# Kernel tuning notes

Hardware: AMD Instinct MI355X
Metric: run time of the kernel (lower is better)

Reference implementation:

```python
import jax, jax.numpy as jnp
import numpy as np

# Dims
B_, L_, IN_ = 16, 8192, 57
DM, DS, HD, EXP, NL, OUT = 64, 32, 32, 2, 2, 6
DI = EXP * DM            # 128 inner dim
NH = DI // HD            # 4 heads
DPROJ = 2 * DI + 2 * DS + NH  # z, x, B, C, dt


def setup_inputs() -> dict:
    key = jax.random.key(0)
    ks = jax.random.split(key, 8)
    def rn(k, shape, scale=0.02):
        return jax.random.normal(k, shape, dtype=jnp.float32) * scale
    return {
        "x": jax.random.normal(ks[0], (B_, L_, IN_), dtype=jnp.float32),
        "W_in": rn(ks[1], (IN_, DM)),
        "b_in": jnp.zeros((DM,), jnp.float32),
        "in_proj_W": rn(ks[2], (NL, DM, DPROJ)),
        "in_proj_b": jnp.zeros((NL, DPROJ), jnp.float32),
        "A_log": jnp.log(jnp.broadcast_to(jnp.arange(1, NH + 1, dtype=jnp.float32), (NL, NH))),
        "D": jnp.ones((NL, NH), jnp.float32),
        "dt_bias": rn(ks[3], (NL, NH), 0.1),
        "out_proj_W": rn(ks[4], (NL, DI, DM)),
        "out_proj_b": jnp.zeros((NL, DM), jnp.float32),
        "cls_W": rn(ks[5], (DM, OUT)),
        "cls_b": jnp.zeros((OUT,), jnp.float32),
    }


def _mamba_layer(x, W, b, A_log, D, dt_bias, Wo, bo):
    """SISO Mamba3-style selective scan block. x: [B, L, DM]."""
    Bsz, L, _ = x.shape
    zxbcdt = x @ W + b                               # [B, L, DPROJ]
    z, xin, Bm, Cm, dt = jnp.split(
        zxbcdt, [DI, 2 * DI, 2 * DI + DS, 2 * DI + 2 * DS], axis=-1)
    dt = jax.nn.softplus(dt + dt_bias)               # [B, L, NH]
    A = -jnp.exp(A_log)                              # [NH], per-head scalar (SISO)
    xin = jax.nn.silu(xin).reshape(Bsz, L, NH, HD)   # [B, L, NH, HD]
    Bm = jax.nn.silu(Bm)                             # [B, L, DS]
    Cm = jax.nn.silu(Cm)                             # [B, L, DS]
    decay = jnp.exp(dt * A)                          # [B, L, NH]

    def step(h, inp):
        # h: [B, NH, HD, DS]
        xt, bt, ct, dtt, dect = inp
        h = dect[:, :, None, None] * h + (dtt[:, :, None] * xt)[..., None] * bt[:, None, None, :]
        yt = jnp.einsum('bhpn,bn->bhp', h, ct)       # [B, NH, HD]
        return h, yt

    h0 = jnp.zeros((Bsz, NH, HD, DS), x.dtype)
    xs = (jnp.moveaxis(xin, 1, 0), jnp.moveaxis(Bm, 1, 0), jnp.moveaxis(Cm, 1, 0),
          jnp.moveaxis(dt, 1, 0), jnp.moveaxis(decay, 1, 0))
    _, ys = jax.lax.scan(step, h0, xs)               # [L, B, NH, HD]
    y = jnp.moveaxis(ys, 0, 1) + D[None, None, :, None] * xin
    y = y.reshape(Bsz, L, DI) * jax.nn.silu(z)       # gated output
    return y @ Wo + bo                               # [B, L, DM]


def reference(x, W_in, b_in, in_proj_W, in_proj_b, A_log, D, dt_bias,
              out_proj_W, out_proj_b, cls_W, cls_b):
    h = x @ W_in + b_in                              # linear_in
    for l in range(NL):                              # residual Mamba stack
        h = h + _mamba_layer(h, in_proj_W[l], in_proj_b[l], A_log[l], D[l],
                             dt_bias[l], out_proj_W[l], out_proj_b[l])
    pooled = h.mean(axis=1)                          # AdaptiveAvgPool1d(1)
    return pooled @ cls_W + cls_b                    # classifier [B, OUT]
```

## Files before the change

kernel.cpp:

```cpp
#include <hip/hip_runtime.h>

#define BSZ   16
#define LSEQ  8192
#define DMDL  64
#define DSD   32
#define HDD   32
#define NHD   4
#define DIN   128
#define NLAY  2
#define NOUTC 6
#define DPRJ  324
#define QC    64
#define NCH   128
#define NT21  21

typedef __attribute__((ext_vector_type(8))) short bf16x8;
typedef __attribute__((ext_vector_type(4))) float f32x4;

__device__ float          g_h0[BSZ*LSEQ*DMDL];
__device__ unsigned short g_xy[BSZ*LSEQ*DIN];
__device__ unsigned short g_Ca[BSZ*LSEQ*DSD];
__device__ float          g_pc[BSZ*LSEQ*NHD];
__device__ unsigned short g_cS[BSZ*NCH*NHD*HDD*DSD];
__device__ unsigned short g_Hb[BSZ*NCH*NHD*HDD*DSD];
__device__ float          g_cL[BSZ*NCH*NHD];
__device__ float          g_ppc[BSZ*NCH*DMDL];
__device__ unsigned short g_wf[NLAY*NT21*2*64*8];
__device__ unsigned short g_wo[NLAY*4*4*64*8];

__device__ __forceinline__ float silu_f(float v){ return v / (1.0f + __expf(-v)); }
__device__ __forceinline__ float softplus_f(float v){ return (v > 15.0f) ? v : __logf(1.0f + __expf(v)); }
__device__ __forceinline__ unsigned short f2bf(float f){
  union { float f; unsigned u; } v; v.f = f;
  unsigned r = v.u + 0x7FFFu + ((v.u >> 16) & 1u);
  return (unsigned short)(r >> 16);
}
__device__ __forceinline__ float bf2f(unsigned short h){
  union { unsigned u; float f; } v; v.u = ((unsigned)h) << 16;
  return v.f;
}
__device__ __forceinline__ unsigned cvtpk(float lo, float hi){
  unsigned r;
  asm("v_cvt_pk_bf16_f32 %0, %1, %2" : "=v"(r) : "v"(lo), "v"(hi));
  return r;
}

#define LSTR 132
__global__ __launch_bounds__(256) void k_linin(
    const float* __restrict__ x, const float* __restrict__ W,
    const float* __restrict__ bias)
{
  __shared__ float xt[57*LSTR];
  __shared__ float wl[57*64];
  const int tid = threadIdx.x;
  const long tb = (long)blockIdx.x * 128;
  for (int i = tid; i < 912; i += 256)
    *(float4*)&wl[i*4] = *(const float4*)&W[i*4];
  for (int i = tid; i < 1824; i += 256){
    float4 v = *(const float4*)&x[tb*57 + (long)i*4];
    const int e = i*4;
    int t0 = e / 57;
    int k0 = e - t0*57;
    float vv[4] = {v.x, v.y, v.z, v.w};
    #pragma unroll
    for (int j = 0; j < 4; ++j){
      int t = t0, k = k0 + j;
      if (k >= 57){ t += 1; k -= 57; }
      xt[k*LSTR + t] = vv[j];
    }
  }
  __syncthreads();
  const int d0 = (tid & 7) * 8;
  const int t0 = (tid >> 3) * 4;
  float acc[4][8];
  #pragma unroll
  for (int i = 0; i < 4; ++i)
    #pragma unroll
    for (int j = 0; j < 8; ++j) acc[i][j] = 0.f;
  #pragma unroll 4
  for (int k = 0; k < 57; ++k){
    float4 xv4 = *(const float4*)&xt[k*LSTR + t0];
    float4 w0  = *(const float4*)&wl[k*64 + d0];
    float4 w1  = *(const float4*)&wl[k*64 + d0 + 4];
    float xv[4] = {xv4.x, xv4.y, xv4.z, xv4.w};
    float wv[8] = {w0.x, w0.y, w0.z, w0.w, w1.x, w1.y, w1.z, w1.w};
    #pragma unroll
    for (int i = 0; i < 4; ++i)
      #pragma unroll
      for (int j = 0; j < 8; ++j) acc[i][j] += xv[i] * wv[j];
  }
  float4 bb0 = *(const float4*)&bias[d0];
  float4 bb1 = *(const float4*)&bias[d0 + 4];
  #pragma unroll
  for (int i = 0; i < 4; ++i){
    float4 o0, o1;
    o0.x = acc[i][0] + bb0.x; o0.y = acc[i][1] + bb0.y;
    o0.z = acc[i][2] + bb0.z; o0.w = acc[i][3] + bb0.w;
    o1.x = acc[i][4] + bb1.x; o1.y = acc[i][5] + bb1.y;
    o1.z = acc[i][6] + bb1.z; o1.w = acc[i][7] + bb1.w;
    *(float4*)&g_h0[(tb + t0 + i)*64 + d0]     = o0;
    *(float4*)&g_h0[(tb + t0 + i)*64 + d0 + 4] = o1;
  }
}

__global__ __launch_bounds__(128) void k_wprep(
    const float* __restrict__ W, const float* __restrict__ Wo)
{
  const int l = blockIdx.y;
  if (blockIdx.x < NT21){
    const int nt = blockIdx.x;
    const int ks = threadIdx.x >> 6, lane = threadIdx.x & 63;
    const float* Wl = W + (long)l*64*DPRJ;
    const int n  = nt*16 + (lane & 15);
    const int k0 = ks*32 + (lane >> 4)*8;
    unsigned short v[8];
    #pragma unroll
    for (int j = 0; j < 8; ++j)
      v[j] = (n < DPRJ) ? f2bf(Wl[(k0 + j)*DPRJ + n]) : (unsigned short)0;
    unsigned short* d = &g_wf[((((long)l*NT21 + nt)*2 + ks)*64 + lane)*8];
    *(ushort4*)&d[0] = make_ushort4(v[0], v[1], v[2], v[3]);
    *(ushort4*)&d[4] = make_ushort4(v[4], v[5], v[6], v[7]);
  } else {
    const int bx = blockIdx.x - NT21;
    if (threadIdx.x >= 64) return;
    const int nt = bx >> 2, ks = bx & 3;
    const int lane = threadIdx.x;
    const int n  = nt*16 + (lane & 15);
    const int k0 = ks*32 + (lane >> 4)*8;
    const float* Wl = Wo + (long)l*128*64;
    unsigned short* d = &g_wo[((((long)l*4 + nt)*4 + ks)*64 + lane)*8];
    unsigned short v[8];
    #pragma unroll
    for (int j = 0; j < 8; ++j) v[j] = f2bf(Wl[(k0 + j)*64 + n]);
    *(ushort4*)&d[0] = make_ushort4(v[0], v[1], v[2], v[3]);
    *(ushort4*)&d[4] = make_ushort4(v[4], v[5], v[6], v[7]);
  }
}

#define SB 40
#define ST 72
__device__ __forceinline__ int xsw(int p, int s){
  return p*ST + (((((s) >> 3) + ((p) >> 2)) & 7) << 3) + ((s) & 7);
}
__device__ __forceinline__ int xsw8(int p, int blk){
  return p*ST + (((((blk)) + ((p) >> 2)) & 7) << 3);
}
__global__ __launch_bounds__(256) void k_ps(
    const float* __restrict__ ipb, const float* __restrict__ dtb,
    const float* __restrict__ A_log, const float* __restrict__ Dp, int l)
{
  __shared__ __align__(16) unsigned short AfrX[4096];
  __shared__ __align__(16) unsigned short U[2*64*SB];
  __shared__ __align__(16) unsigned short Bbt[32*ST];
  __shared__ __align__(16) unsigned short Xt0[32*ST];
  __shared__ __align__(16) unsigned short Mb0[64*ST];
  __shared__ float Sl[4*64];
  __shared__ float dts[4*64];
  __shared__ float wls[4*64];
  const int tid = threadIdx.x;
  const int cI = blockIdx.x, b = blockIdx.y;
  const long tb = (long)b*LSEQ + (long)cI*QC;
  const long bc = (long)b*NCH + cI;
  unsigned short* Bb = U;
  unsigned short* Cb = U + 64*SB;
  unsigned short* Mb1 = U;
  float* etl = (float*)&AfrX[2304];
  float* esd = (float*)&AfrX[2816];
  for (int i = tid; i < 512; i += 256){
    const int t = i >> 3, k8 = i & 7;
    float4 f0 = *(const float4*)&g_h0[(tb + t)*64 + k8*8];
    float4 f1 = *(const float4*)&g_h0[(tb + t)*64 + k8*8 + 4];
    const int mt = t >> 4, ks = k8 >> 2, q = k8 & 3, ln = (t & 15) + 16*q;
    uint4 pk;
    pk.x = cvtpk(f0.x, f0.y); pk.y = cvtpk(f0.z, f0.w);
    pk.z = cvtpk(f1.x, f1.y); pk.w = cvtpk(f1.z, f1.w);
    *(uint4*)&AfrX[(((mt*2 + ks)*64) + ln)*8] = pk;
  }
  __syncthreads();
  const int w = tid >> 6, lane = tid & 63;
  const int colq = lane & 15, rowq = lane >> 4;
  const int t4 = w*16 + rowq*4;
  const float* bl = ipb + (long)l*DPRJ;
  const unsigned short* wf = &g_wf[(long)l*NT21*2*64*8];
  const bf16x8 a0 = *(const bf16x8*)&AfrX[((w*2 + 0)*64 + lane)*8];
  const bf16x8 a1 = *(const bf16x8*)&AfrX[((w*2 + 1)*64 + lane)*8];
  #pragma unroll
  for (int nti = 0; nti < 2; ++nti){
    const int nt = 16 + nti;
    bf16x8 b0 = *(const bf16x8*)&wf[((nt*2 + 0)*64 + lane)*8];
    bf16x8 b1 = *(const bf16x8*)&wf[((nt*2 + 1)*64 + lane)*8];
    const float bia = bl[nt*16 + colq];
    f32x4 acc = {0.f, 0.f, 0.f, 0.f};
    acc = __builtin_amdgcn_mfma_f32_16x16x32_bf16(a0, b0, acc, 0, 0, 0);
    acc = __builtin_amdgcn_mfma_f32_16x16x32_bf16(a1, b1, acc, 0, 0, 0);
    const unsigned u0 = cvtpk(silu_f(acc[0] + bia), silu_f(acc[1] + bia));
    const unsigned u1 = cvtpk(silu_f(acc[2] + bia), silu_f(acc[3] + bia));
    const int n = nti*16 + colq;
    uint2 uu; uu.x = u0; uu.y = u1;
    *(uint2*)&Bbt[xsw(n, t4)] = uu;
    Bb[(t4 + 0)*SB + n] = (unsigned short)(u0 & 0xFFFFu);
    Bb[(t4 + 1)*SB + n] = (unsigned short)(u0 >> 16);
    Bb[(t4 + 2)*SB + n] = (unsigned short)(u1 & 0xFFFFu);
    Bb[(t4 + 3)*SB + n] = (unsigned short)(u1 >> 16);
  }
  #pragma unroll
  for (int nti = 0; nti < 2; ++nti){
    const int nt = 18 + nti;
    bf16x8 b0 = *(const bf16x8*)&wf[((nt*2 + 0)*64 + lane)*8];
    bf16x8 b1 = *(const bf16x8*)&wf[((nt*2 + 1)*64 + lane)*8];
    f32x4 acc = {0.f, 0.f, 0.f, 0.f};
    acc = __builtin_amdgcn_mfma_f32_16x16x32_bf16(b0, a0, acc, 0, 0, 0);
    acc = __builtin_amdgcn_mfma_f32_16x16x32_bf16(b1, a1, acc, 0, 0, 0);
    float4 bia4 = *(const float4*)&bl[nt*16 + rowq*4];
    uint2 uu;
    uu.x = cvtpk(silu_f(acc[0] + bia4.x), silu_f(acc[1] + bia4.y));
    uu.y = cvtpk(silu_f(acc[2] + bia4.z), silu_f(acc[3] + bia4.w));
    *(uint2*)&Cb[(w*16 + colq)*SB + nti*16 + rowq*4] = uu;
  }
  {
    bf16x8 b0 = *(const bf16x8*)&wf[((20*2 + 0)*64 + lane)*8];
    bf16x8 b1 = *(const bf16x8*)&wf[((20*2 + 1)*64 + lane)*8];
    f32x4 acc = {0.f, 0.f, 0.f, 0.f};
    acc = __builtin_amdgcn_mfma_f32_16x16x32_bf16(b0, a0, acc, 0, 0, 0);
    acc = __builtin_amdgcn_mfma_f32_16x16x32_bf16(b1, a1, acc, 0, 0, 0);
    if (rowq == 0){
      float4 bia4 = *(const float4*)&bl[320];
      float4 dtb4 = *(const float4*)&dtb[l*4];
      const int t = w*16 + colq;
      dts[0*64 + t] = softplus_f(acc[0] + (bia4.x + dtb4.x));
      dts[1*64 + t] = softplus_f(acc[1] + (bia4.y + dtb4.y));
      dts[2*64 + t] = softplus_f(acc[2] + (bia4.z + dtb4.z));
      dts[3*64 + t] = softplus_f(acc[3] + (bia4.w + dtb4.w));
    }
  }
  __syncthreads();
  {
    const int h = w, t = lane;
    const float Ah = -__expf(A_log[l*4 + h]);
    const float v = dts[h*64 + t];
    float x = v * Ah;
    #pragma unroll
    for (int d = 1; d < 64; d <<= 1){
      float y = __shfl_up(x, d);
      if (t >= d) x += y;
    }
    Sl[h*64 + t] = x;
    const float send = __shfl(x, 63);
    wls[h*64 + t] = __expf(send - x) * v;
    if (t == 63) g_cL[(bc)*4 + h] = x;
    g_pc[(tb + t)*4 + h] = __expf(x);
    const float bA = __shfl(x, 0), bB = __shfl(x, 16);
    const float bC = __shfl(x, 32), bD = __shfl(x, 48);
    const int tt = t >> 4;
    const float bt = (tt == 0) ? bA : ((tt == 1) ? bB : ((tt == 2) ? bC : bD));
    etl[h*64 + t] = __expf(x - bt);
    if (t < 16) esd[h*96 + t]      = __expf(bB - x) * v;
    if (t < 32) esd[h*96 + 16 + t] = __expf(bC - x) * v;
    if (t < 48) esd[h*96 + 48 + t] = __expf(bD - x) * v;
  }
  {
    const int t = tid >> 2, c0 = (tid & 3) * 8;
    *(uint4*)&g_Ca[(tb + t)*32 + c0] = *(const uint4*)&Cb[t*SB + c0];
  }
  float Greg[3][4];
  int Gmt[3], Gst[3];
  #pragma unroll
  for (int rep = 0; rep < 3; ++rep){
    const int k = w + rep*4;
    if (k < 10){
      const int mt = (k >= 6) ? 3 : ((k >= 3) ? 2 : ((k >= 1) ? 1 : 0));
      const int st = k - mt*(mt+1)/2;
      Gmt[rep] = mt; Gst[rep] = st;
      bf16x8 af = *(const bf16x8*)&Bb[(st*16 + colq)*SB + rowq*8];
      bf16x8 bf = *(const bf16x8*)&Cb[(mt*16 + colq)*SB + rowq*8];
      f32x4 acc = {0.f, 0.f, 0.f, 0.f};
      acc = __builtin_amdgcn_mfma_f32_16x16x32_bf16(af, bf, acc, 0, 0, 0);
      #pragma unroll
      for (int r = 0; r < 4; ++r) Greg[rep][r] = acc[r];
    } else { Gmt[rep] = -1; Gst[rep] = 0; }
  }
  #pragma unroll
  for (int rep = 0; rep < 2; ++rep){
    const int k = w + rep*4;
    if (k < 6){
      const int mt = (k < 3) ? 0 : ((k < 5) ? 1 : 2);
      const int st = (k < 3) ? (k + 1) : ((k < 5) ? (k - 1) : 3);
      uint2 zz; zz.x = 0; zz.y = 0;
      *(uint2*)&Mb0[xsw(mt*16 + colq, st*16 + rowq*4)] = zz;
    }
  }
  bf16x8 cw0, cw1, cw2, cw3;
  float cbia0, cbia1;
  cw0 = *(const bf16x8*)&wf[((8*2 + 0)*64 + lane)*8];
  cw1 = *(const bf16x8*)&wf[((8*2 + 1)*64 + lane)*8];
  cw2 = *(const bf16x8*)&wf[((9*2 + 0)*64 + lane)*8];
  cw3 = *(const bf16x8*)&wf[((9*2 + 1)*64 + lane)*8];
  cbia0 = bl[8*16 + colq];
  cbia1 = bl[9*16 + colq];
  __syncthreads();
  for (int h = 0; h < NHD; ++h){
    unsigned short* Xt  = (h & 1) ? AfrX : Xt0;
    unsigned short* Mbh = (h & 1) ? Mb1 : Mb0;
    {
      f32x4 acc = {0.f, 0.f, 0.f, 0.f};
      acc = __builtin_amdgcn_mfma_f32_16x16x32_bf16(a0, cw0, acc, 0, 0, 0);
      acc = __builtin_amdgcn_mfma_f32_16x16x32_bf16(a1, cw1, acc, 0, 0, 0);
      uint2 uu;
      uu.x = cvtpk(silu_f(acc[0] + cbia0), silu_f(acc[1] + cbia0));
      uu.y = cvtpk(silu_f(acc[2] + cbia0), silu_f(acc[3] + cbia0));
      *(uint2*)&Xt[xsw(colq, t4)] = uu;
    }
    {
      f32x4 acc = {0.f, 0.f, 0.f, 0.f};
      acc = __builtin_amdgcn_mfma_f32_16x16x32_bf16(a0, cw2, acc, 0, 0, 0);
      acc = __builtin_amdgcn_mfma_f32_16x16x32_bf16(a1, cw3, acc, 0, 0, 0);
      uint2 uu;
      uu.x = cvtpk(silu_f(acc[0] + cbia1), silu_f(acc[1] + cbia1));
      uu.y = cvtpk(silu_f(acc[2] + cbia1), silu_f(acc[3] + cbia1));
      *(uint2*)&Xt[xsw(16 + colq, t4)] = uu;
    }
    const int hn = (h + 1) & 3;
    bf16x8 nw0 = *(const bf16x8*)&wf[(((8 + 2*hn)*2 + 0)*64 + lane)*8];
    bf16x8 nw1 = *(const bf16x8*)&wf[(((8 + 2*hn)*2 + 1)*64 + lane)*8];
    bf16x8 nw2 = *(const bf16x8*)&wf[(((9 + 2*hn)*2 + 0)*64 + lane)*8];
    bf16x8 nw3 = *(const bf16x8*)&wf[(((9 + 2*hn)*2 + 1)*64 + lane)*8];
    const float nbia0 = bl[(8 + 2*hn)*16 + colq];
    const float nbia1 = bl[(9 + 2*hn)*16 + colq];
    if (h == 1){
      #pragma unroll
      for (int rep = 0; rep < 2; ++rep){
        const int k = w + rep*4;
        if (k < 6){
          const int mt = (k < 3) ? 0 : ((k < 5) ? 1 : 2);
          const int st = (k < 3) ? (k + 1) : ((k < 5) ? (k - 1) : 3);
          uint2 zz; zz.x = 0; zz.y = 0;
          *(uint2*)&Mb1[xsw(mt*16 + colq, st*16 + rowq*4)] = zz;
        }
      }
    }
    #pragma unroll
    for (int rep = 0; rep < 3; ++rep){
      if (Gmt[rep] >= 0){
        const int mt = Gmt[rep], st = Gst[rep];
        const int t = mt*16 + colq;
        const int s0 = st*16 + rowq*4;
        float m0, m1, m2, m3;
        if (st < mt){
          const float et = etl[h*64 + t];
          const int off = (mt == 1) ? 0 : ((mt == 2) ? 16 : 48);
          float4 e4 = *(const float4*)&esd[h*96 + off + s0];
          m0 = et * e4.x * Greg[rep][0];
          m1 = et * e4.y * Greg[rep][1];
          m2 = et * e4.z * Greg[rep][2];
          m3 = et * e4.w * Greg[rep][3];
        } else {
          const float slt = Sl[h*64 + t];
          float4 s4 = *(const float4*)&Sl[h*64 + s0];
          float4 d4 = *(const float4*)&dts[h*64 + s0];
          m0 = (s0 + 0 <= t) ? __expf(slt - s4.x) * d4.x * Greg[rep][0] : 0.f;
          m1 = (s0 + 1 <= t) ? __expf(slt - s4.y) * d4.y * Greg[rep][1] : 0.f;
          m2 = (s0 + 2 <= t) ? __expf(slt - s4.z) * d4.z * Greg[rep][2] : 0.f;
          m3 = (s0 + 3 <= t) ? __expf(slt - s4.w) * d4.w * Greg[rep][3] : 0.f;
        }
        uint2 uu;
        uu.x = cvtpk(m0, m1);
        uu.y = cvtpk(m2, m3);
        *(uint2*)&Mbh[xsw(t, s0)] = uu;
      }
    }
    __syncthreads();
    __builtin_amdgcn_s_setprio(1);
    const float Dh = Dp[l*4 + h];
    bf16x8 ma0 = *(const bf16x8*)&Mbh[xsw8(w*16 + colq, rowq)];
    bf16x8 ma1 = *(const bf16x8*)&Mbh[xsw8(w*16 + colq, rowq + 4)];
    bf16x8 xb0, xb1;
    const int tcol = w*16 + colq;
    #pragma unroll
    for (int nt = 0; nt < 2; ++nt){
      bf16x8 b0 = *(const bf16x8*)&Xt[xsw8(nt*16 + colq, rowq)];
      bf16x8 b1 = *(const bf16x8*)&Xt[xsw8(nt*16 + colq, rowq + 4)];
      if (nt == (w & 1)){ xb0 = b0; xb1 = b1; }
      f32x4 acc = {0.f, 0.f, 0.f, 0.f};
      acc = __builtin_amdgcn_mfma_f32_16x16x32_bf16(b0, ma0, acc, 0, 0, 0);
      acc = __builtin_amdgcn_mfma_f32_16x16x32_bf16(b1, ma1, acc, 0, 0, 0);
      const int p0 = nt*16 + rowq*4;
      float yv[4];
      #pragma unroll
      for (int r = 0; r < 4; ++r)
        yv[r] = acc[r] + Dh * bf2f(Xt[xsw(p0 + r, tcol)]);
      uint2 uu;
      uu.x = cvtpk(yv[0], yv[1]);
      uu.y = cvtpk(yv[2], yv[3]);
      const long ybase = ((((bc*NHD + h)*4 + w)*2 + nt)*256);
      *(uint2*)&g_xy[ybase + lane*4] = uu;
    }
    {
      union { bf16x8 v; unsigned short us[8]; } sx0, sx1;
      union { bf16x8 v; unsigned u[4]; } sa0, sa1;
      sx0.v = xb0; sx1.v = xb1;
      #pragma unroll
      for (int jj = 0; jj < 4; ++jj){
        sa0.u[jj] = cvtpk(bf2f(sx0.us[2*jj])   * wls[h*64 + rowq*8 + 2*jj],
                          bf2f(sx0.us[2*jj+1]) * wls[h*64 + rowq*8 + 2*jj + 1]);
        sa1.u[jj] = cvtpk(bf2f(sx1.us[2*jj])   * wls[h*64 + 32 + rowq*8 + 2*jj],
                          bf2f(sx1.us[2*jj+1]) * wls[h*64 + 32 + rowq*8 + 2*jj + 1]);
      }
      const int mt = w & 1, nt2 = w >> 1;
      bf16x8 bb0 = *(const bf16x8*)&Bbt[xsw8(nt2*16 + colq, rowq)];
      bf16x8 bb1 = *(const bf16x8*)&Bbt[xsw8(nt2*16 + colq, rowq + 4)];
      f32x4 acc = {0.f, 0.f, 0.f, 0.f};
      acc = __builtin_amdgcn_mfma_f32_16x16x32_bf16(sa0.v, bb0, acc, 0, 0, 0);
      acc = __builtin_amdgcn_mfma_f32_16x16x32_bf16(sa1.v, bb1, acc, 0, 0, 0);
      const long base = ((bc*NHD + h))*(long)(HDD*DSD);
      const int n = nt2*16 + colq;
      #pragma unroll
      for (int r = 0; r < 4; ++r){
        const int p = mt*16 + rowq*4 + r;
        g_cS[base + p*32 + n] = f2bf(acc[r]);
      }
    }
    __builtin_amdgcn_s_setprio(0);
    cw0 = nw0; cw1 = nw1; cw2 = nw2; cw3 = nw3;
    cbia0 = nbia0; cbia1 = nbia1;
  }
}

__global__ __launch_bounds__(128) void k_s2()
{
  const int h = blockIdx.x >> 3, seg = blockIdx.x & 7, b = blockIdx.y;
  const int idx = seg*128 + threadIdx.x;
  float H = 0.f;
  #pragma unroll 4
  for (int c = 0; c < NCH; ++c){
    const long o = (((long)b*NCH + c)*NHD + h)*1024 + idx;
    const float cs = bf2f(g_cS[o]);
    const float lg = g_cL[((long)b*NCH + c)*4 + h];
    g_Hb[o] = f2bf(H);
    H = __expf(lg) * H + cs;
  }
}

__global__ __launch_bounds__(256) void k_s3(
    const float* __restrict__ ipb, const float* __restrict__ bo, int l, int finalLayer)
{
  __shared__ __align__(16) unsigned short Hb[128*40];
  __shared__ __align__(16) unsigned short Cb[64*40];
  __shared__ __align__(16) unsigned short gl[64*136];
  __shared__ float pcl[4*64];
  __shared__ float csum[4*64];
  const int tid = threadIdx.x;
  const int cI = blockIdx.x, b = blockIdx.y;
  const long tb = (long)b*LSEQ + (long)cI*QC;
  const long bc = (long)b*NCH + cI;
  const long hbase = (bc*NHD)*(long)(HDD*DSD);
  for (int i = tid; i < 512; i += 256){
    const int hp = i >> 2, n0 = (i & 3) * 8;
    *(uint4*)&Hb[hp*40 + n0] = *(const uint4*)&g_Hb[hbase + hp*32 + n0];
  }
  for (int i = tid; i < 512; i += 256){
    const int t = i >> 3, n0 = (i & 7) * 4;
    *(ushort4*)&Cb[t*40 + n0] = *(const ushort4*)&g_Ca[(tb + t)*32 + n0];
  }
  { int t = tid >> 2, h = tid & 3; pcl[h*64 + t] = g_pc[(tb + t)*4 + h]; }
  __syncthreads();
  const int w = tid >> 6, lane = tid & 63;
  const int colq = lane & 15, rowq = lane >> 4;
  const float* blz = ipb + (long)l*DPRJ;
  const unsigned short* wfz = &g_wf[(long)l*NT21*2*64*8];
  {
    const long tok0 = tb + w*16 + colq;
    bf16x8 h0a, h0b;
    {
      float4 f0 = *(const float4*)&g_h0[tok0*64 + rowq*8];
      float4 f1 = *(const float4*)&g_h0[tok0*64 + rowq*8 + 4];
      float4 f2 = *(const float4*)&g_h0[tok0*64 + 32 + rowq*8];
      float4 f3 = *(const float4*)&g_h0[tok0*64 + 32 + rowq*8 + 4];
      union { bf16x8 v; unsigned u[4]; } ca, cb2;
      ca.u[0] = cvtpk(f0.x, f0.y); ca.u[1] = cvtpk(f0.z, f0.w);
      ca.u[2] = cvtpk(f1.x, f1.y); ca.u[3] = cvtpk(f1.z, f1.w);
      cb2.u[0] = cvtpk(f2.x, f2.y); cb2.u[1] = cvtpk(f2.z, f2.w);
      cb2.u[2] = cvtpk(f3.x, f3.y); cb2.u[3] = cvtpk(f3.z, f3.w);
      h0a = ca.v; h0b = cb2.v;
    }
    bf16x8 a = *(const bf16x8*)&Cb[(w*16 + colq)*40 + rowq*8];
    const int tcol = w*16 + colq;
    #pragma unroll
    for (int nt = 0; nt < 8; ++nt){
      bf16x8 bfr = *(const bf16x8*)&Hb[(nt*16 + colq)*40 + rowq*8];
      f32x4 acc = {0.f, 0.f, 0.f, 0.f};
      acc = __builtin_amdgcn_mfma_f32_16x16x32_bf16(bfr, a, acc, 0, 0, 0);
      bf16x8 bz0 = *(const bf16x8*)&wfz[((nt*2 + 0)*64 + lane)*8];
      bf16x8 bz1 = *(const bf16x8*)&wfz[((nt*2 + 1)*64 + lane)*8];
      f32x4 zac = {0.f, 0.f, 0.f, 0.f};
      zac = __builtin_amdgcn_mfma_f32_16x16x32_bf16(bz0, h0a, zac, 0, 0, 0);
      zac = __builtin_amdgcn_mfma_f32_16x16x32_bf16(bz1, h0b, zac, 0, 0, 0);
      const int h = nt >> 1, ntp = nt & 1;
      const int hp0 = nt*16 + rowq*4;
      float4 zb4 = *(const float4*)&blz[hp0];
      const float pcv = pcl[h*64 + tcol];
      const ushort4 yv = *(const ushort4*)&g_xy[(((bc*NHD + h)*4 + w)*2 + ntp)*256 + lane*4];
      const float g0 = (pcv * acc[0] + bf2f(yv.x)) * silu_f(zac[0] + zb4.x);
      const float g1 = (pcv * acc[1] + bf2f(yv.y)) * silu_f(zac[1] + zb4.y);
      const float g2 = (pcv * acc[2] + bf2f(yv.z)) * silu_f(zac[2] + zb4.z);
      const float g3 = (pcv * acc[3] + bf2f(yv.w)) * silu_f(zac[3] + zb4.w);
      uint2 uu;
      uu.x = cvtpk(g0, g1);
      uu.y = cvtpk(g2, g3);
      *(uint2*)&gl[tcol*136 + hp0] = uu;
    }
  }
  __syncthreads();
  const unsigned short* wo = &g_wo[(long)l*4*4*512];
  #pragma unroll
  for (int nt2 = 0; nt2 < 4; ++nt2){
    f32x4 acc = {0.f, 0.f, 0.f, 0.f};
    #pragma unroll
    for (int ks = 0; ks < 4; ++ks){
      bf16x8 a = *(const bf16x8*)&gl[(w*16 + colq)*136 + ks*32 + rowq*8];
      bf16x8 bfr = *(const bf16x8*)&wo[(nt2*4 + ks)*512 + lane*8];
      acc = __builtin_amdgcn_mfma_f32_16x16x32_bf16(a, bfr, acc, 0, 0, 0);
    }
    const int dm = nt2*16 + colq;
    const float bb = bo[l*64 + dm];
    float part = 0.f;
    #pragma unroll
    for (int r = 0; r < 4; ++r){
      const int t = w*16 + rowq*4 + r;
      const long tok = tb + t;
      const float o = acc[r] + bb + g_h0[tok*64 + dm];
      g_h0[tok*64 + dm] = o;
      part += o;
    }
    if (finalLayer){
      part += __shfl_xor(part, 16);
      part += __shfl_xor(part, 32);
      if (rowq == 0) csum[w*64 + dm] = part;
    }
  }
  if (finalLayer){
    __syncthreads();
    if (tid < 64){
      g_ppc[((long)b*NCH + cI)*64 + tid] =
        csum[tid] + csum[64 + tid] + csum[128 + tid] + csum[192 + tid];
    }
  }
}

__global__ __launch_bounds__(64) void k_pool2(
    const float* __restrict__ cW, const float* __restrict__ cb,
    float* __restrict__ out)
{
  __shared__ float pl[64];
  const int b = blockIdx.x, tid = threadIdx.x;
  float s = 0.f;
  for (int c = 0; c < NCH; ++c) s += g_ppc[((long)b*NCH + c)*64 + tid];
  pl[tid] = s * (1.0f / 8192.0f);
  __syncthreads();
  if (tid < NOUTC){
    float acc = cb[tid];
    for (int dm = 0; dm < 64; ++dm) acc += pl[dm] * cW[dm*NOUTC + tid];
    out[b*NOUTC + tid] = acc;
  }
}

extern "C" void kernel_launch(void* const* d_in, const int* in_sizes, int n_in,
                              void* d_out, int out_size, void* d_ws, size_t ws_size,
                              hipStream_t stream)
{
  const float* x      = (const float*)d_in[0];
  const float* W_in   = (const float*)d_in[1];
  const float* b_in   = (const float*)d_in[2];
  const float* ipW    = (const float*)d_in[3];
  const float* ipb    = (const float*)d_in[4];
  const float* A_log  = (const float*)d_in[5];
  const float* Dp     = (const float*)d_in[6];
  const float* dtb    = (const float*)d_in[7];
  const float* opW    = (const float*)d_in[8];
  const float* opb    = (const float*)d_in[9];
  const float* clsW   = (const float*)d_in[10];
  const float* clsb   = (const float*)d_in[11];
  float* out = (float*)d_out;
  (void)d_ws; (void)ws_size;

  k_wprep<<<dim3(NT21 + 16, NLAY), 128, 0, stream>>>(ipW, opW);
  k_linin<<<1024, 256, 0, stream>>>(x, W_in, b_in);
  for (int l = 0; l < NLAY; ++l){
    k_ps<<<dim3(NCH, BSZ), 256, 0, stream>>>(ipb, dtb, A_log, Dp, l);
    k_s2<<<dim3(32, BSZ), 128, 0, stream>>>();
    k_s3<<<dim3(NCH, BSZ), 256, 0, stream>>>(ipb, opb, l, (l == NLAY-1) ? 1 : 0);
  }
  k_pool2<<<BSZ, 64, 0, stream>>>(clsW, clsb, out);
}
```

Measured before the change: 290.5 us.

## Split inter-chunk state scan into segmented two-level scan

The serial 128-chunk state recurrence becomes a two-level scan. Eight segments of 16 chunks are scanned in parallel, a small kernel then propagates carries across the segments, and k_s3 folds the carried state, scaled by the cumulative decay, into the chunk start states as it loads them. This gives the scan eight times more blocks and shortens the serial dependency chain, at the cost of an extra launch, extra float state traffic, and slightly different rounding because the bf16 partial state is added to a float correction.

```diff
diff --git a/kernel.cpp b/kernel.cpp
--- a/kernel.cpp
+++ b/kernel.cpp
@@ -12,6 +12,7 @@
 #define DPRJ  324
 #define QC    64
 #define NCH   128
+#define NSEG  8
 #define NT21  21
 
 typedef __attribute__((ext_vector_type(8))) short bf16x8;
@@ -24,6 +25,10 @@
 __device__ unsigned short g_cS[BSZ*NCH*NHD*HDD*DSD];
 __device__ unsigned short g_Hb[BSZ*NCH*NHD*HDD*DSD];
 __device__ float          g_cL[BSZ*NCH*NHD];
+__device__ float          g_Hs [BSZ*NSEG*NHD*1024];
+__device__ float          g_Hst[BSZ*NSEG*NHD*1024];
+__device__ float          g_pd [BSZ*NCH*NHD];
+__device__ float          g_pds[BSZ*NSEG*NHD];
 __device__ float          g_ppc[BSZ*NCH*DMDL];
 __device__ unsigned short g_wf[NLAY*NT21*2*64*8];
 __device__ unsigned short g_wo[NLAY*4*4*64*8];
@@ -425,18 +430,39 @@
   }
 }
 
-__global__ __launch_bounds__(128) void k_s2()
-{
-  const int h = blockIdx.x >> 3, seg = blockIdx.x & 7, b = blockIdx.y;
-  const int idx = seg*128 + threadIdx.x;
-  float H = 0.f;
+__global__ __launch_bounds__(128) void k_s2a()
+{
+  const int h = blockIdx.x >> 3, iseg = blockIdx.x & 7;
+  const int b = blockIdx.y, cseg = blockIdx.z;
+  const int idx = iseg*128 + threadIdx.x;
+  float H = 0.f, S = 0.f;
   #pragma unroll 4
-  for (int c = 0; c < NCH; ++c){
+  for (int cc = 0; cc < 16; ++cc){
+    const int c = cseg*16 + cc;
     const long o = (((long)b*NCH + c)*NHD + h)*1024 + idx;
     const float cs = bf2f(g_cS[o]);
     const float lg = g_cL[((long)b*NCH + c)*4 + h];
     g_Hb[o] = f2bf(H);
-    H = __expf(lg) * H + cs;
+    if (iseg == 0 && threadIdx.x == 0)
+      g_pd[((long)b*NCH + c)*4 + h] = __expf(S);
+    H = __expf(lg)*H + cs;
+    S += lg;
+  }
+  g_Hs[(((long)b*NSEG + cseg)*NHD + h)*1024 + idx] = H;
+  if (iseg == 0 && threadIdx.x == 0)
+    g_pds[((long)b*NSEG + cseg)*4 + h] = __expf(S);
+}
+
+__global__ __launch_bounds__(128) void k_s2b()
+{
+  const int h = blockIdx.x >> 3, iseg = blockIdx.x & 7, b = blockIdx.y;
+  const int idx = iseg*128 + threadIdx.x;
+  float Hs = 0.f;
+  #pragma unroll
+  for (int cseg = 0; cseg < NSEG; ++cseg){
+    const long o = (((long)b*NSEG + cseg)*NHD + h)*1024 + idx;
+    g_Hst[o] = Hs;
+    Hs = g_pds[((long)b*NSEG + cseg)*4 + h]*Hs + g_Hs[o];
   }
 }
 
@@ -453,9 +479,20 @@
   const long tb = (long)b*LSEQ + (long)cI*QC;
   const long bc = (long)b*NCH + cI;
   const long hbase = (bc*NHD)*(long)(HDD*DSD);
+  const long hsb = (((long)b*NSEG + (cI >> 4))*NHD)*1024;
   for (int i = tid; i < 512; i += 256){
     const int hp = i >> 2, n0 = (i & 3) * 8;
-    *(uint4*)&Hb[hp*40 + n0] = *(const uint4*)&g_Hb[hbase + hp*32 + n0];
+    const float pd = g_pd[bc*4 + (hp >> 5)];
+    union { uint4 q; unsigned short us[8]; } u;
+    u.q = *(const uint4*)&g_Hb[hbase + hp*32 + n0];
+    float4 s0 = *(const float4*)&g_Hst[hsb + hp*32 + n0];
+    float4 s1 = *(const float4*)&g_Hst[hsb + hp*32 + n0 + 4];
+    uint4 q;
+    q.x = cvtpk(bf2f(u.us[0]) + pd*s0.x, bf2f(u.us[1]) + pd*s0.y);
+    q.y = cvtpk(bf2f(u.us[2]) + pd*s0.z, bf2f(u.us[3]) + pd*s0.w);
+    q.z = cvtpk(bf2f(u.us[4]) + pd*s1.x, bf2f(u.us[5]) + pd*s1.y);
+    q.w = cvtpk(bf2f(u.us[6]) + pd*s1.z, bf2f(u.us[7]) + pd*s1.w);
+    *(uint4*)&Hb[hp*40 + n0] = q;
   }
   for (int i = tid; i < 512; i += 256){
     const int t = i >> 3, n0 = (i & 7) * 4;
@@ -586,7 +623,8 @@
   k_linin<<<1024, 256, 0, stream>>>(x, W_in, b_in);
   for (int l = 0; l < NLAY; ++l){
     k_ps<<<dim3(NCH, BSZ), 256, 0, stream>>>(ipb, dtb, A_log, Dp, l);
-    k_s2<<<dim3(32, BSZ), 128, 0, stream>>>();
+    k_s2a<<<dim3(32, BSZ, NSEG), 128, 0, stream>>>();
+    k_s2b<<<dim3(32, BSZ), 128, 0, stream>>>();
     k_s3<<<dim3(NCH, BSZ), 256, 0, stream>>>(ipb, opb, l, (l == NLAY-1) ? 1 : 0);
   }
   k_pool2<<<BSZ, 64, 0, stream>>>(clsW, clsb, out);
```

Result: no change. 286.2 us (-1.5%).
